# Kernel optimization log

Hardware: AMD Instinct MI355X
Metric: run time of the kernel (lower is better)

Reference implementation:

```python
import jax, jax.numpy as jnp
import numpy as np

DIM = 1024
D_STATE = 16
D_CONV = 4
EXPAND = 2
D_INNER = EXPAND * DIM          # 2048
DT_RANK = (DIM + 15) // 16      # 64 (math.ceil(d_model/16))
BSZ = 2
SEQ = 2048


def setup_inputs() -> dict:
    key = jax.random.key(0)
    ks = jax.random.split(key, 8)
    g = lambda k, shape, scale: (jax.random.normal(k, shape, jnp.float32) * scale)
    return {
        "x": g(ks[0], (BSZ, SEQ, DIM), 1.0),
        # in_proj: Linear(d_model -> 2*d_inner, bias=False)
        "W_in": g(ks[1], (2 * D_INNER, DIM), DIM ** -0.5),
        # depthwise causal conv1d: groups=d_inner, kernel d_conv, bias=True
        "conv_w": g(ks[2], (D_INNER, 1, D_CONV), D_CONV ** -0.5),
        "conv_b": jnp.zeros((D_INNER,), jnp.float32),
        # x_proj: Linear(d_inner -> dt_rank + 2*d_state, bias=False)
        "W_xproj": g(ks[3], (DT_RANK + 2 * D_STATE, D_INNER), D_INNER ** -0.5),
        # dt_proj: Linear(dt_rank -> d_inner, bias=True)
        "W_dt": g(ks[4], (D_INNER, DT_RANK), DT_RANK ** -0.5),
        "b_dt": g(ks[5], (D_INNER,), 0.1),
        # S4D-real init: A = -exp(A_log), A_log = log(1..d_state)
        "A_log": jnp.log(jnp.broadcast_to(
            jnp.arange(1, D_STATE + 1, dtype=jnp.float32), (D_INNER, D_STATE))),
        "D": jnp.ones((D_INNER,), jnp.float32),
        # out_proj: Linear(d_inner -> d_model, bias=False)
        "W_out": g(ks[6], (DIM, D_INNER), D_INNER ** -0.5),
        # wrapper LayerNorm(dim)
        "gamma": jnp.ones((DIM,), jnp.float32),
        "beta": jnp.zeros((DIM,), jnp.float32),
    }


def reference(x, W_in, conv_w, conv_b, W_xproj, W_dt, b_dt,
              A_log, D, W_out, gamma, beta):
    B, L, _ = x.shape
    # ---- input projection, split into conv path and gate ----
    xz = x @ W_in.T                              # (B, L, 2*d_inner)
    xc, z = jnp.split(xz, 2, axis=-1)
    # ---- depthwise causal conv1d + SiLU ----
    xt = jnp.transpose(xc, (0, 2, 1))            # (B, d_inner, L)
    conv = jax.lax.conv_general_dilated(
        xt, conv_w, window_strides=(1,), padding=[(D_CONV - 1, 0)],
        dimension_numbers=("NCH", "OIH", "NCH"), feature_group_count=D_INNER)
    u = jax.nn.silu(jnp.transpose(conv + conv_b[None, :, None], (0, 2, 1)))  # (B,L,d_inner)
    # ---- input-dependent delta, B, C ----
    xdbc = u @ W_xproj.T                          # (B, L, dt_rank + 2*d_state)
    dt = xdbc[..., :DT_RANK]
    Bm = xdbc[..., DT_RANK:DT_RANK + D_STATE]     # (B, L, d_state)
    Cm = xdbc[..., DT_RANK + D_STATE:]            # (B, L, d_state)
    delta = jax.nn.softplus(dt @ W_dt.T + b_dt)   # (B, L, d_inner)
    A = -jnp.exp(A_log)                           # (d_inner, d_state)
    # ---- selective scan: h_t = exp(dt*A) h_{t-1} + dt*B_t*u_t ; y_t = <h_t, C_t> ----
    def step(h, inputs):
        d_t, u_t, B_t, C_t = inputs               # (B,d_inner),(B,d_inner),(B,S),(B,S)
        dA = jnp.exp(d_t[:, :, None] * A)         # (B, d_inner, S)
        h = h * dA + (d_t * u_t)[:, :, None] * B_t[:, None, :]
        y = jnp.einsum("bds,bs->bd", h, C_t)
        return h, y
    tm = lambda a: jnp.transpose(a, (1, 0, 2))    # time-major for scan
    h0 = jnp.zeros((B, D_INNER, D_STATE), x.dtype)
    _, ys = jax.lax.scan(step, h0, (tm(delta), tm(u), tm(Bm), tm(Cm)))
    y = jnp.transpose(ys, (1, 0, 2)) + u * D      # skip term D*u
    y = y * jax.nn.silu(z)                        # gate
    out = y @ W_out.T                             # (B, L, dim)
    # ---- wrapper LayerNorm(dim), eps=1e-5 ----
    mean = out.mean(-1, keepdims=True)
    var = out.var(-1, keepdims=True)
    return (out - mean) * jax.lax.rsqrt(var + 1e-5) * gamma + beta
```

## Files before the change

### kernel.cpp

```cpp
#include <hip/hip_runtime.h>
#include <stdint.h>

typedef unsigned short u16;
typedef __bf16 bf16x8 __attribute__((ext_vector_type(8)));
typedef unsigned short u16x8 __attribute__((ext_vector_type(8)));
typedef unsigned short u16x4 __attribute__((ext_vector_type(4)));
typedef float f32x4 __attribute__((ext_vector_type(4)));

#define BSZ 2
#define SEQ 2048
#define DIM 1024
#define D_INNER 2048
#define DT_RANK 64
#define D_STATE 16
#define XPROJ_N 96
#define NCHUNK 32
#define CHUNK_T 64
#define LOG2E 1.44269504f

#define N_X   4194304
#define N_W   4194304
#define N_WX  196608
#define N_WDT 131072
#define N_WO  2097152
#define N_XD  393216

__device__ __forceinline__ float bf2f(u16 h) {
    return __uint_as_float(((unsigned)h) << 16);
}
__device__ __forceinline__ u16 f2bf(float f) {
    unsigned u = __float_as_uint(f);
    unsigned r = (u + 0x7FFFu + ((u >> 16) & 1u)) >> 16;
    return (u16)r;
}

__device__ __forceinline__ f32x4 mfma16(bf16x8 a, bf16x8 b, f32x4 c) {
    return __builtin_amdgcn_mfma_f32_16x16x32_bf16(a, b, c, 0, 0, 0);
}

__device__ __forceinline__ void gload_lds16(const void* g, void* l) {
    __builtin_amdgcn_global_load_lds(
        (const __attribute__((address_space(1))) unsigned int*)(uintptr_t)g,
        (__attribute__((address_space(3))) unsigned int*)(uintptr_t)l,
        16, 0, 0);
}

__device__ __forceinline__ void split4(const float* __restrict__ in,
                                       u16* __restrict__ hi, u16* __restrict__ lo,
                                       long i)
{
    f32x4 v = *(const f32x4*)(in + i);
    u16x4 h, l;
    #pragma unroll
    for (int j = 0; j < 4; j++) {
        u16 hh = f2bf(v[j]);
        h[j] = hh;
        l[j] = f2bf(v[j] - bf2f(hh));
    }
    *(u16x4*)(hi + i) = h;
    *(u16x4*)(lo + i) = l;
}

__global__ __launch_bounds__(256)
void megasplit4(const float* __restrict__ x,  u16* __restrict__ xh,  u16* __restrict__ xl,
                const float* __restrict__ w,  u16* __restrict__ wh,  u16* __restrict__ wl,
                const float* __restrict__ wx, u16* __restrict__ wxh, u16* __restrict__ wxl,
                const float* __restrict__ wd, u16* __restrict__ wdh, u16* __restrict__ wdl)
{
    long i = ((long)blockIdx.x * 256 + threadIdx.x) * 4;
    if (i < N_X) { split4(x, xh, xl, i); return; }
    i -= N_X;
    if (i < N_W) { split4(w, wh, wl, i); return; }
    i -= N_W;
    if (i < N_WX) { split4(wx, wxh, wxl, i); return; }
    i -= N_WX;
    if (i < N_WDT) { split4(wd, wdh, wdl, i); }
}

#define PH_TOP                                                                \
    __builtin_amdgcn_sched_barrier(0);                                        \
    __builtin_amdgcn_s_barrier();                                             \
    asm volatile("s_waitcnt lgkmcnt(0)" ::: "memory");                        \
    __builtin_amdgcn_sched_barrier(0);                                        \
    __builtin_amdgcn_s_setprio(1);
#define PH_BOT                                                                \
    __builtin_amdgcn_s_setprio(0);                                            \
    __builtin_amdgcn_sched_barrier(0);                                        \
    __builtin_amdgcn_s_barrier();

__global__ __launch_bounds__(512, 2)
void gemm256_xz(const u16* __restrict__ xh, const u16* __restrict__ xl,
                const u16* __restrict__ wh, const u16* __restrict__ wl,
                u16* __restrict__ xc, float* __restrict__ z)
{
    __shared__ u16 lds[65536];

    const int tid  = threadIdx.x;
    const int w    = tid >> 6;
    const int lane = tid & 63;
    const int r16  = lane & 15;
    const int quad = lane >> 4;
    const int wr   = w >> 2;
    const int wc   = w & 3;
    const long m0  = (long)blockIdx.y * 256;
    const long n0  = (long)blockIdx.x * 256;

    const int c0 = tid, c1 = tid + 512;
    const int ma0 = c0 >> 2, kc0 = ((c0 & 3) ^ ((ma0 >> 1) & 3)) * 8;
    const int ma1 = c1 >> 2, kc1 = ((c1 & 3) ^ ((ma1 >> 1) & 3)) * 8;
    const int arow0 = ((int)m0 + ma0) * DIM + kc0;
    const int arow1 = ((int)m0 + ma1) * DIM + kc1;
    const int brow0 = ((int)n0 + ma0) * DIM + kc0;
    const int brow1 = ((int)n0 + ma1) * DIM + kc1;

    int caof[8], cbof[4];
    #pragma unroll
    for (int i = 0; i < 8; i++) {
        int m = wr * 128 + i * 16 + r16;
        caof[i] = (m * 4 + (quad ^ ((m >> 1) & 3))) * 8;
    }
    #pragma unroll
    for (int j = 0; j < 4; j++) {
        int n = wc * 64 + j * 16 + r16;
        cbof[j] = (n * 4 + (quad ^ ((n >> 1) & 3))) * 8;
    }

    f32x4 acc[8][4];
    #pragma unroll
    for (int i = 0; i < 8; i++)
        #pragma unroll
        for (int j = 0; j < 4; j++) acc[i][j] = {0.f, 0.f, 0.f, 0.f};

    gload_lds16(xh + arow0, lds + c0 * 8);
    gload_lds16(xh + arow1, lds + c1 * 8);
    gload_lds16(xl + arow0, lds + 8192 + c0 * 8);
    gload_lds16(xl + arow1, lds + 8192 + c1 * 8);
    gload_lds16(wh + brow0, lds + 16384 + c0 * 8);
    gload_lds16(wh + brow1, lds + 16384 + c1 * 8);
    gload_lds16(wl + brow0, lds + 24576 + c0 * 8);
    gload_lds16(wl + brow1, lds + 24576 + c1 * 8);
    asm volatile("s_waitcnt vmcnt(0)" ::: "memory");
    __builtin_amdgcn_s_barrier();

    int kt = 0;
#define XZ_FTILE(CUR, SN)                                                     \
  {                                                                           \
    int st = kt + 1; if (st > 31) st = 31;                                    \
    const int kb = st * 32;                                                   \
    const u16* AHp = lds + (CUR) * 32768;                                     \
    const u16* ALp = AHp + 8192;                                              \
    const u16* BHp = AHp + 16384;                                             \
    const u16* BLp = AHp + 24576;                                             \
    u16* Sb = lds + (SN) * 32768;                                             \
    bf16x8 a0[4], a1[4], fb[4];                                               \
                            \
    _Pragma("unroll") for (int j = 0; j < 4; j++)                             \
        fb[j] = *(const bf16x8*)(BHp + cbof[j]);                              \
    _Pragma("unroll") for (int i = 0; i < 4; i++)                             \
        a0[i] = *(const bf16x8*)(AHp + caof[i]);                              \
    gload_lds16(xh + arow0 + kb, Sb + c0 * 8);                                \
    gload_lds16(xh + arow1 + kb, Sb + c1 * 8);                                \
    PH_TOP                                                                    \
    _Pragma("unroll") for (int i = 0; i < 4; i++)                             \
      _Pragma("unroll") for (int j = 0; j < 4; j++)                           \
        acc[i][j] = mfma16(a0[i], fb[j], acc[i][j]);                          \
    PH_BOT                                                                    \
                                \
    _Pragma("unroll") for (int i = 0; i < 4; i++)                             \
        a1[i] = *(const bf16x8*)(AHp + caof[4 + i]);                          \
    gload_lds16(xl + arow0 + kb, Sb + 8192 + c0 * 8);                         \
    gload_lds16(xl + arow1 + kb, Sb + 8192 + c1 * 8);                         \
    PH_TOP                                                                    \
    _Pragma("unroll") for (int i = 0; i < 4; i++)                             \
      _Pragma("unroll") for (int j = 0; j < 4; j++)                           \
        acc[4 + i][j] = mfma16(a1[i], fb[j], acc[4 + i][j]);                  \
    PH_BOT                                                                    \
                        \
    _Pragma("unroll") for (int j = 0; j < 4; j++)                             \
        fb[j] = *(const bf16x8*)(BLp + cbof[j]);                              \
    gload_lds16(wh + brow0 + kb, Sb + 16384 + c0 * 8);                        \
    gload_lds16(wh + brow1 + kb, Sb + 16384 + c1 * 8);                        \
    PH_TOP                                                                    \
    _Pragma("unroll") for (int i = 0; i < 4; i++)                             \
      _Pragma("unroll") for (int j = 0; j < 4; j++)                           \
        acc[i][j] = mfma16(a0[i], fb[j], acc[i][j]);                          \
    PH_BOT                                                                    \
                             \
    gload_lds16(wl + brow0 + kb, Sb + 24576 + c0 * 8);                        \
    gload_lds16(wl + brow1 + kb, Sb + 24576 + c1 * 8);                        \
    PH_TOP                                                                    \
    _Pragma("unroll") for (int i = 0; i < 4; i++)                             \
      _Pragma("unroll") for (int j = 0; j < 4; j++)                           \
        acc[4 + i][j] = mfma16(a1[i], fb[j], acc[4 + i][j]);                  \
    PH_BOT                                                                    \
                              \
    _Pragma("unroll") for (int j = 0; j < 4; j++)                             \
        fb[j] = *(const bf16x8*)(BHp + cbof[j]);                              \
    _Pragma("unroll") for (int i = 0; i < 4; i++)                             \
        a0[i] = *(const bf16x8*)(ALp + caof[i]);                              \
    PH_TOP                                                                    \
    _Pragma("unroll") for (int i = 0; i < 4; i++)                             \
      _Pragma("unroll") for (int j = 0; j < 4; j++)                           \
        acc[i][j] = mfma16(a0[i], fb[j], acc[i][j]);                          \
    PH_BOT                                                                    \
                 \
    _Pragma("unroll") for (int i = 0; i < 4; i++)                             \
        a1[i] = *(const bf16x8*)(ALp + caof[4 + i]);                          \
    PH_TOP                                                                    \
    _Pragma("unroll") for (int i = 0; i < 4; i++)                             \
      _Pragma("unroll") for (int j = 0; j < 4; j++)                           \
        acc[4 + i][j] = mfma16(a1[i], fb[j], acc[4 + i][j]);                  \
    __builtin_amdgcn_s_setprio(0);                                            \
    __builtin_amdgcn_sched_barrier(0);                                        \
    asm volatile("s_waitcnt vmcnt(0)" ::: "memory");                          \
    __builtin_amdgcn_s_barrier();                                             \
    kt++;                                                                     \
  }

    #pragma unroll 1
    for (int it = 0; it < 16; it++) {
        XZ_FTILE(0, 1)
        XZ_FTILE(1, 0)
    }
#undef XZ_FTILE

    asm volatile("s_waitcnt vmcnt(0)" ::: "memory");

    const bool isz = (n0 >= 2048);
    #pragma unroll
    for (int i = 0; i < 8; i++) {
        #pragma unroll
        for (int j = 0; j < 4; j++) {
            long col = n0 + wc * 64 + j * 16 + r16;
            #pragma unroll
            for (int r = 0; r < 4; r++) {
                long row = m0 + wr * 128 + i * 16 + quad * 4 + r;
                if (!isz) xc[row * (long)D_INNER + col] = f2bf(acc[i][j][r]);
                else      z[row * (long)D_INNER + (col - D_INNER)] = acc[i][j][r];
            }
        }
    }
}

__global__ __launch_bounds__(512, 2)
void gemm256_out(const u16* __restrict__ A, const u16* __restrict__ Bh,
                 const u16* __restrict__ Bl, float* __restrict__ OutBase)
{
    __shared__ u16 lds[49152];

    const int tid  = threadIdx.x;
    const int w    = tid >> 6;
    const int lane = tid & 63;
    const int r16  = lane & 15;
    const int quad = lane >> 4;
    const int wr   = w >> 2;
    const int wc   = w & 3;
    const long m0  = (long)blockIdx.y * 256;
    const long n0  = (long)blockIdx.x * 256;
    const int  kz  = blockIdx.z;
    const u16* Bs  = (kz >= 2) ? Bl : Bh;
    const int  kbase = (kz & 1) * 1024;
    float* Out = OutBase + (long)kz * 4194304;

    const int c0 = tid, c1 = tid + 512;
    const int ma0 = c0 >> 2, kc0 = ((c0 & 3) ^ ((ma0 >> 1) & 3)) * 8;
    const int ma1 = c1 >> 2, kc1 = ((c1 & 3) ^ ((ma1 >> 1) & 3)) * 8;
    const int arow0 = ((int)m0 + ma0) * D_INNER + kbase + kc0;
    const int arow1 = ((int)m0 + ma1) * D_INNER + kbase + kc1;
    const int brow0 = ((int)n0 + ma0) * D_INNER + kbase + kc0;
    const int brow1 = ((int)n0 + ma1) * D_INNER + kbase + kc1;

    int caof[8], cbof[4];
    #pragma unroll
    for (int i = 0; i < 8; i++) {
        int m = wr * 128 + i * 16 + r16;
        caof[i] = (m * 4 + (quad ^ ((m >> 1) & 3))) * 8;
    }
    #pragma unroll
    for (int j = 0; j < 4; j++) {
        int n = wc * 64 + j * 16 + r16;
        cbof[j] = (n * 4 + (quad ^ ((n >> 1) & 3))) * 8;
    }

    f32x4 acc[8][4];
    #pragma unroll
    for (int i = 0; i < 8; i++)
        #pragma unroll
        for (int j = 0; j < 4; j++) acc[i][j] = {0.f, 0.f, 0.f, 0.f};

    gload_lds16(A  + arow0,      lds + c0 * 8);
    gload_lds16(A  + arow1,      lds + c1 * 8);
    gload_lds16(Bs + brow0,      lds + 24576 + c0 * 8);
    gload_lds16(Bs + brow1,      lds + 24576 + c1 * 8);
    gload_lds16(A  + arow0 + 32, lds + 8192 + c0 * 8);
    gload_lds16(A  + arow1 + 32, lds + 8192 + c1 * 8);
    gload_lds16(Bs + brow0 + 32, lds + 24576 + 8192 + c0 * 8);
    gload_lds16(Bs + brow1 + 32, lds + 24576 + 8192 + c1 * 8);
    asm volatile("s_waitcnt vmcnt(4)" ::: "memory");
    __builtin_amdgcn_s_barrier();

    int kt = 0;
#define OUT_ITER(CUR, SL)                                                     \
  {                                                                           \
    int st = kt + 2; if (st > 31) st = 31;                                    \
    const int kb = st * 32;                                                   \
    const u16* Alds = lds + (CUR) * 8192;                                     \
    const u16* Blds = lds + 24576 + (CUR) * 8192;                             \
    bf16x8 bfr[4], afr[4];                                                    \
    _Pragma("unroll") for (int j = 0; j < 4; j++)                             \
        bfr[j] = *(const bf16x8*)(Blds + cbof[j]);                            \
    _Pragma("unroll") for (int i = 0; i < 4; i++)                             \
        afr[i] = *(const bf16x8*)(Alds + caof[i]);                            \
    gload_lds16(A + arow0 + kb, lds + (SL) * 8192 + c0 * 8);                  \
    gload_lds16(A + arow1 + kb, lds + (SL) * 8192 + c1 * 8);                  \
    PH_TOP                                                                    \
    _Pragma("unroll") for (int i = 0; i < 4; i++)                             \
      _Pragma("unroll") for (int j = 0; j < 4; j++)                           \
        acc[i][j] = mfma16(afr[i], bfr[j], acc[i][j]);                        \
    PH_BOT                                                                    \
    bf16x8 af2[4];                                                            \
    _Pragma("unroll") for (int i = 0; i < 4; i++)                             \
        af2[i] = *(const bf16x8*)(Alds + caof[4 + i]);                        \
    gload_lds16(Bs + brow0 + kb, lds + 24576 + (SL) * 8192 + c0 * 8);         \
    gload_lds16(Bs + brow1 + kb, lds + 24576 + (SL) * 8192 + c1 * 8);         \
    PH_TOP                                                                    \
    _Pragma("unroll") for (int i = 0; i < 4; i++)                             \
      _Pragma("unroll") for (int j = 0; j < 4; j++)                           \
        acc[4 + i][j] = mfma16(af2[i], bfr[j], acc[4 + i][j]);                \
    __builtin_amdgcn_s_setprio(0);                                            \
    __builtin_amdgcn_sched_barrier(0);                                        \
    asm volatile("s_waitcnt vmcnt(4)" ::: "memory");                          \
    __builtin_amdgcn_s_barrier();                                             \
    kt++;                                                                     \
  }

    #pragma unroll 1
    for (int it = 0; it < 10; it++) {
        OUT_ITER(0, 2)
        OUT_ITER(1, 0)
        OUT_ITER(2, 1)
    }
    OUT_ITER(0, 2)
    OUT_ITER(1, 0)
#undef OUT_ITER

    asm volatile("s_waitcnt vmcnt(0)" ::: "memory");

    #pragma unroll
    for (int i = 0; i < 8; i++) {
        #pragma unroll
        for (int j = 0; j < 4; j++) {
            long col = n0 + wc * 64 + j * 16 + r16;
            #pragma unroll
            for (int r = 0; r < 4; r++) {
                long row = m0 + wr * 128 + i * 16 + quad * 4 + r;
                Out[row * (long)DIM + col] = acc[i][j][r];
            }
        }
    }
}

__global__ __launch_bounds__(64)
void gemm_dt32(const u16* __restrict__ Ah, const u16* __restrict__ Al, int lda,
               const u16* __restrict__ Bh, const u16* __restrict__ Bl, int ldb,
               float* __restrict__ C, int ldc, const float* __restrict__ bias)
{
    const int lane = threadIdx.x;
    const int r16  = lane & 15;
    const int quad = lane >> 4;
    const long m0 = (long)blockIdx.y * 32;
    const long n0 = (long)blockIdx.x * 32;

    const u16* Ah0 = Ah + (m0 + r16) * (long)lda + quad * 8;
    const u16* Ah1 = Ah0 + 16L * lda;
    const u16* Al0 = Al + (m0 + r16) * (long)lda + quad * 8;
    const u16* Al1 = Al0 + 16L * lda;
    const u16* Bh0 = Bh + (n0 + r16) * (long)ldb + quad * 8;
    const u16* Bh1 = Bh0 + 16L * ldb;
    const u16* Bl0 = Bl + (n0 + r16) * (long)ldb + quad * 8;
    const u16* Bl1 = Bl0 + 16L * ldb;

    f32x4 acc00 = {0,0,0,0}, acc01 = {0,0,0,0}, acc10 = {0,0,0,0}, acc11 = {0,0,0,0};

    #pragma unroll
    for (int k = 0; k < DT_RANK; k += 32) {
        bf16x8 a0h = *(const bf16x8*)(Ah0 + k);
        bf16x8 a1h = *(const bf16x8*)(Ah1 + k);
        bf16x8 a0l = *(const bf16x8*)(Al0 + k);
        bf16x8 a1l = *(const bf16x8*)(Al1 + k);
        bf16x8 b0h = *(const bf16x8*)(Bh0 + k);
        bf16x8 b1h = *(const bf16x8*)(Bh1 + k);
        bf16x8 b0l = *(const bf16x8*)(Bl0 + k);
        bf16x8 b1l = *(const bf16x8*)(Bl1 + k);
        acc00 = mfma16(a0h, b0h, acc00); acc00 = mfma16(a0h, b0l, acc00); acc00 = mfma16(a0l, b0h, acc00);
        acc01 = mfma16(a0h, b1h, acc01); acc01 = mfma16(a0h, b1l, acc01); acc01 = mfma16(a0l, b1h, acc01);
        acc10 = mfma16(a1h, b0h, acc10); acc10 = mfma16(a1h, b0l, acc10); acc10 = mfma16(a1l, b0h, acc10);
        acc11 = mfma16(a1h, b1h, acc11); acc11 = mfma16(a1h, b1l, acc11); acc11 = mfma16(a1l, b1h, acc11);
    }

    #pragma unroll
    for (int i = 0; i < 2; i++) {
        #pragma unroll
        for (int j = 0; j < 2; j++) {
            f32x4 v = (i == 0) ? (j == 0 ? acc00 : acc01) : (j == 0 ? acc10 : acc11);
            long col = n0 + j * 16 + r16;
            #pragma unroll
            for (int r = 0; r < 4; r++) {
                long row = m0 + i * 16 + quad * 4 + r;
                float x = v[r] + bias[col];
                x = (x > 15.f) ? x : log1pf(__expf(x));
                C[row * (long)ldc + col] = x;
            }
        }
    }
}

__global__ __launch_bounds__(64)
void gemm3_skp(const u16* __restrict__ A, int lda,
               const u16* __restrict__ Bh, const u16* __restrict__ Bl, int ldb,
               float* __restrict__ Cpart, int ldc, int K0)
{
    const int lane = threadIdx.x;
    const int r16  = lane & 15;
    const int quad = lane >> 4;
    const long m0 = (long)blockIdx.y * 32;
    const long n0 = (long)blockIdx.x * 32;
    const int kbase = blockIdx.z * K0;
    float* C = Cpart + (long)blockIdx.z * N_XD;

    const u16* Ap0 = A  + (m0 + r16) * (long)lda + quad * 8 + kbase;
    const u16* Ap1 = Ap0 + 16L * lda;
    const u16* Bh0 = Bh + (n0 + r16) * (long)ldb + quad * 8 + kbase;
    const u16* Bh1 = Bh0 + 16L * ldb;
    const u16* Bl0 = Bl + (n0 + r16) * (long)ldb + quad * 8 + kbase;
    const u16* Bl1 = Bl0 + 16L * ldb;

    f32x4 acc00 = {0,0,0,0}, acc01 = {0,0,0,0}, acc10 = {0,0,0,0}, acc11 = {0,0,0,0};

    for (int k = 0; k < K0; k += 32) {
        bf16x8 a0 = *(const bf16x8*)(Ap0 + k);
        bf16x8 a1 = *(const bf16x8*)(Ap1 + k);
        bf16x8 b0h = *(const bf16x8*)(Bh0 + k);
        bf16x8 b1h = *(const bf16x8*)(Bh1 + k);
        bf16x8 b0l = *(const bf16x8*)(Bl0 + k);
        bf16x8 b1l = *(const bf16x8*)(Bl1 + k);
        acc00 = mfma16(a0, b0h, acc00); acc00 = mfma16(a0, b0l, acc00);
        acc01 = mfma16(a0, b1h, acc01); acc01 = mfma16(a0, b1l, acc01);
        acc10 = mfma16(a1, b0h, acc10); acc10 = mfma16(a1, b0l, acc10);
        acc11 = mfma16(a1, b1h, acc11); acc11 = mfma16(a1, b1l, acc11);
    }

    #pragma unroll
    for (int i = 0; i < 2; i++) {
        #pragma unroll
        for (int j = 0; j < 2; j++) {
            f32x4 v = (i == 0) ? (j == 0 ? acc00 : acc01) : (j == 0 ? acc10 : acc11);
            long col = n0 + j * 16 + r16;
            #pragma unroll
            for (int r = 0; r < 4; r++) {
                long row = m0 + i * 16 + quad * 4 + r;
                C[row * (long)ldc + col] = v[r];
            }
        }
    }
}

__global__ __launch_bounds__(256)
void combine3(const float* __restrict__ part, float* __restrict__ xdbc,
              u16* __restrict__ hi, u16* __restrict__ lo)
{
    long i = ((long)blockIdx.x * 256 + threadIdx.x) * 4;
    if (i >= N_XD) return;
    f32x4 s = *(const f32x4*)(part + i);
    #pragma unroll
    for (int j = 1; j < 8; j++) {
        f32x4 p = *(const f32x4*)(part + (long)j * N_XD + i);
        s[0] += p[0]; s[1] += p[1]; s[2] += p[2]; s[3] += p[3];
    }
    *(f32x4*)(xdbc + i) = s;
    u16x4 h, l;
    #pragma unroll
    for (int j = 0; j < 4; j++) {
        u16 hh = f2bf(s[j]);
        h[j] = hh;
        l[j] = f2bf(s[j] - bf2f(hh));
    }
    *(u16x4*)(hi + i) = h;
    *(u16x4*)(lo + i) = l;
}

__global__ __launch_bounds__(256)
void conv_silu(const u16* __restrict__ xc, const float* __restrict__ cw,
               const float* __restrict__ cb, u16* __restrict__ u)
{
    long idx = ((long)blockIdx.x * 256 + threadIdx.x) * 8;
    int t  = (int)((idx >> 11) & 2047);
    int d0 = (int)(idx & 2047);

    bf16x8 xrow[4];
    #pragma unroll
    for (int j = 0; j < 4; j++) {
        int tt = t - 3 + j;
        if (tt >= 0) xrow[j] = *(const bf16x8*)(xc + idx + (long)(j - 3) * D_INNER);
        else         xrow[j] = bf16x8{0,0,0,0,0,0,0,0};
    }
    u16x8 out;
    #pragma unroll
    for (int e = 0; e < 8; e++) {
        int d = d0 + e;
        float acc = cb[d];
        #pragma unroll
        for (int j = 0; j < 4; j++)
            acc += cw[d * 4 + j] * (float)xrow[j][e];
        out[e] = f2bf(acc / (1.f + __expf(-acc)));
    }
    *(u16x8*)(u + idx) = out;
}

__global__ __launch_bounds__(256)
void scan_partA(const float* __restrict__ delta, const u16* __restrict__ u,
                const float* __restrict__ xdbc, const float* __restrict__ A_log,
                float* __restrict__ hbuf, float* __restrict__ sdelta,
                const float* __restrict__ wout, u16* __restrict__ wouth,
                u16* __restrict__ woutl)
{
    const int d = blockIdx.x * 256 + threadIdx.x;
    const int c = blockIdx.y;
    const int b = blockIdx.z;
    const int t0 = c * CHUNK_T;

    float Af[16];
    #pragma unroll
    for (int s = 0; s < 16; s++) Af[s] = -__expf(A_log[d * 16 + s]) * LOG2E;

    float h[16];
    #pragma unroll
    for (int s = 0; s < 16; s++) h[s] = 0.f;
    float sd = 0.f;

    const float* dptr = delta + ((long)b * SEQ + t0) * D_INNER + d;
    const u16*   uptr = u     + ((long)b * SEQ + t0) * D_INNER + d;
    const float* xp   = xdbc  + ((long)b * SEQ + t0) * XPROJ_N;

    for (int t = 0; t < CHUNK_T; t++) {
        float dl = dptr[(long)t * D_INNER];
        float uu = bf2f(uptr[(long)t * D_INNER]);
        f32x4 B0 = *(const f32x4*)(xp + t * XPROJ_N + DT_RANK);
        f32x4 B1 = *(const f32x4*)(xp + t * XPROJ_N + DT_RANK + 4);
        f32x4 B2 = *(const f32x4*)(xp + t * XPROJ_N + DT_RANK + 8);
        f32x4 B3 = *(const f32x4*)(xp + t * XPROJ_N + DT_RANK + 12);
        float Bv[16] = {B0[0],B0[1],B0[2],B0[3], B1[0],B1[1],B1[2],B1[3],
                        B2[0],B2[1],B2[2],B2[3], B3[0],B3[1],B3[2],B3[3]};
        sd += dl;
        float dlu = dl * uu;
        #pragma unroll
        for (int s = 0; s < 16; s++)
            h[s] = h[s] * exp2f(dl * Af[s]) + dlu * Bv[s];
    }

    float* hout = hbuf + ((long)(b * NCHUNK + c) * D_INNER + d) * 16;
    #pragma unroll
    for (int s = 0; s < 16; s++) hout[s] = h[s];
    sdelta[(long)(b * NCHUNK + c) * D_INNER + d] = sd;

    long tidg = (((long)b * NCHUNK + c) * 8 + blockIdx.x) * 256 + threadIdx.x;
    long base = tidg * 16;
    #pragma unroll
    for (int k = 0; k < 4; k++) split4(wout, wouth, woutl, base + 4 * k);
}

__global__ __launch_bounds__(256)
void scan_fixup(float* __restrict__ hbuf, const float* __restrict__ sdelta,
                const float* __restrict__ A_log)
{
    const int idx = blockIdx.x * 256 + threadIdx.x;
    const int ds = idx & (D_INNER * 16 - 1);
    const int b  = idx >> 15;
    const float Af = -__expf(A_log[ds]) * LOG2E;
    float hin = 0.f;
    #pragma unroll 4
    for (int c = 0; c < NCHUNK; c++) {
        long gi = (long)(b * NCHUNK + c) * (D_INNER * 16) + ds;
        float e = hbuf[gi];
        hbuf[gi] = hin;
        float sd = sdelta[(long)(b * NCHUNK + c) * D_INNER + (ds >> 4)];
        hin = e + exp2f(Af * sd) * hin;
    }
}

__global__ __launch_bounds__(256)
void scan_partC(const float* __restrict__ delta, const u16* __restrict__ u,
                const float* __restrict__ xdbc, const float* __restrict__ z,
                const float* __restrict__ A_log, const float* __restrict__ Dp,
                const float* __restrict__ hbuf, u16* __restrict__ y)
{
    const int d = blockIdx.x * 256 + threadIdx.x;
    const int c = blockIdx.y;
    const int b = blockIdx.z;
    const int t0 = c * CHUNK_T;

    float Af[16];
    #pragma unroll
    for (int s = 0; s < 16; s++) Af[s] = -__expf(A_log[d * 16 + s]) * LOG2E;
    const float Dd = Dp[d];

    float h[16];
    const float* hin = hbuf + ((long)(b * NCHUNK + c) * D_INNER + d) * 16;
    #pragma unroll
    for (int s = 0; s < 16; s++) h[s] = hin[s];

    const float* dptr = delta + ((long)b * SEQ + t0) * D_INNER + d;
    const u16*   uptr = u     + ((long)b * SEQ + t0) * D_INNER + d;
    const float* zptr = z     + ((long)b * SEQ + t0) * D_INNER + d;
    const float* xp   = xdbc  + ((long)b * SEQ + t0) * XPROJ_N;
    u16* yptr = y + ((long)b * SEQ + t0) * D_INNER + d;

    for (int t = 0; t < CHUNK_T; t++) {
        float dl = dptr[(long)t * D_INNER];
        float uu = bf2f(uptr[(long)t * D_INNER]);
        float zl = zptr[(long)t * D_INNER];
        f32x4 B0 = *(const f32x4*)(xp + t * XPROJ_N + DT_RANK);
        f32x4 B1 = *(const f32x4*)(xp + t * XPROJ_N + DT_RANK + 4);
        f32x4 B2 = *(const f32x4*)(xp + t * XPROJ_N + DT_RANK + 8);
        f32x4 B3 = *(const f32x4*)(xp + t * XPROJ_N + DT_RANK + 12);
        f32x4 C0 = *(const f32x4*)(xp + t * XPROJ_N + DT_RANK + 16);
        f32x4 C1 = *(const f32x4*)(xp + t * XPROJ_N + DT_RANK + 20);
        f32x4 C2 = *(const f32x4*)(xp + t * XPROJ_N + DT_RANK + 24);
        f32x4 C3 = *(const f32x4*)(xp + t * XPROJ_N + DT_RANK + 28);
        float Bv[16] = {B0[0],B0[1],B0[2],B0[3], B1[0],B1[1],B1[2],B1[3],
                        B2[0],B2[1],B2[2],B2[3], B3[0],B3[1],B3[2],B3[3]};
        float Cv[16] = {C0[0],C0[1],C0[2],C0[3], C1[0],C1[1],C1[2],C1[3],
                        C2[0],C2[1],C2[2],C2[3], C3[0],C3[1],C3[2],C3[3]};
        float dlu = dl * uu;
        float p0 = 0.f, p1 = 0.f, p2 = 0.f, p3 = 0.f;
        #pragma unroll
        for (int s = 0; s < 16; s += 4) {
            h[s]   = h[s]   * exp2f(dl * Af[s])   + dlu * Bv[s];
            h[s+1] = h[s+1] * exp2f(dl * Af[s+1]) + dlu * Bv[s+1];
            h[s+2] = h[s+2] * exp2f(dl * Af[s+2]) + dlu * Bv[s+2];
            h[s+3] = h[s+3] * exp2f(dl * Af[s+3]) + dlu * Bv[s+3];
            p0 += h[s]   * Cv[s];
            p1 += h[s+1] * Cv[s+1];
            p2 += h[s+2] * Cv[s+2];
            p3 += h[s+3] * Cv[s+3];
        }
        float acc = (p0 + p1) + (p2 + p3);
        float sz = zl / (1.f + __expf(-zl));
        float yy = (acc + uu * Dd) * sz;
        yptr[(long)t * D_INNER] = f2bf(yy);
    }
}

__global__ __launch_bounds__(256)
void layernorm_kernel(const float* __restrict__ p0,
                      const float* __restrict__ gamma, const float* __restrict__ beta,
                      float* __restrict__ out)
{
    const long row = blockIdx.x;
    const long base = row * DIM;
    int tid = threadIdx.x;
    float v[4];
    float sum = 0.f, sq = 0.f;
    #pragma unroll
    for (int i = 0; i < 4; i++) {
        long c = base + tid + i * 256;
        v[i] = (p0[c] + p0[c + 4194304]) + (p0[c + 8388608] + p0[c + 12582912]);
        sum += v[i];
        sq  += v[i] * v[i];
    }
    #pragma unroll
    for (int off = 1; off < 64; off <<= 1) {
        sum += __shfl_xor(sum, off);
        sq  += __shfl_xor(sq, off);
    }
    __shared__ float ssum[4], ssq[4];
    int w = tid >> 6;
    if ((tid & 63) == 0) { ssum[w] = sum; ssq[w] = sq; }
    __syncthreads();
    float ts = ssum[0] + ssum[1] + ssum[2] + ssum[3];
    float tq = ssq[0] + ssq[1] + ssq[2] + ssq[3];
    float mean = ts * (1.f / DIM);
    float var  = tq * (1.f / DIM) - mean * mean;
    float rstd = rsqrtf(var + 1e-5f);
    float* o = out + base;
    #pragma unroll
    for (int i = 0; i < 4; i++) {
        int c = tid + i * 256;
        o[c] = (v[i] - mean) * rstd * gamma[c] + beta[c];
    }
}

extern "C" void kernel_launch(void* const* d_in, const int* in_sizes, int n_in,
                              void* d_out, int out_size, void* d_ws, size_t ws_size,
                              hipStream_t stream)
{
    const float* x      = (const float*)d_in[0];
    const float* W_in   = (const float*)d_in[1];
    const float* conv_w = (const float*)d_in[2];
    const float* conv_b = (const float*)d_in[3];
    const float* W_xproj= (const float*)d_in[4];
    const float* W_dt   = (const float*)d_in[5];
    const float* b_dt   = (const float*)d_in[6];
    const float* A_log  = (const float*)d_in[7];
    const float* Dv     = (const float*)d_in[8];
    const float* W_out  = (const float*)d_in[9];
    const float* gamma  = (const float*)d_in[10];
    const float* beta   = (const float*)d_in[11];

    char* ws = (char*)d_ws;
    u16*   xc    = (u16*)(ws);
    float* g3p   = (float*)(ws);
    u16*   xdh   = (u16*)(ws + 12582912);
    u16*   xdl   = (u16*)(ws + 14155776);
    float* hbuf  = (float*)(ws);
    u16*   wouth = (u16*)(ws + 8388608);
    u16*   woutl = (u16*)(ws + 12582912);
    float* z     = (float*)(ws + 16777216);
    float* opre  = (float*)(ws + 16777216);
    u16*   u     = (u16*)(ws + 50331648);
    u16*   xh    = (u16*)(ws + 67108864);
    u16*   xl    = (u16*)(ws + 75497472);
    u16*   wh    = (u16*)(ws + 83886080);
    u16*   wl    = (u16*)(ws + 92274688);
    float* delta = (float*)(ws + 67108864);
    float* xdbc  = (float*)(ws + 100663296);
    u16*   wxh   = (u16*)(ws + 102236160);
    u16*   wxl   = (u16*)(ws + 102629376);
    u16*   wdth  = (u16*)(ws + 103022592);
    u16*   wdtl  = (u16*)(ws + 103284736);
    float* sdel  = (float*)(ws + 103546880);
    u16*   yb    = (u16*)d_out;

    megasplit4<<<8512, 256, 0, stream>>>(x, xh, xl, W_in, wh, wl,
                                         W_xproj, wxh, wxl, W_dt, wdth, wdtl);
    gemm256_xz<<<dim3(16, 16), 512, 0, stream>>>(xh, xl, wh, wl, xc, z);
    conv_silu<<<4096, 256, 0, stream>>>(xc, conv_w, conv_b, u);
    gemm3_skp<<<dim3(3, 128, 8), 64, 0, stream>>>(
        u, D_INNER, wxh, wxl, D_INNER, g3p, XPROJ_N, 256);
    combine3<<<384, 256, 0, stream>>>(g3p, xdbc, xdh, xdl);
    gemm_dt32<<<dim3(64, 128), 64, 0, stream>>>(
        xdh, xdl, XPROJ_N, wdth, wdtl, DT_RANK, delta, D_INNER, b_dt);
    scan_partA<<<dim3(8, NCHUNK, BSZ), 256, 0, stream>>>(
        delta, u, xdbc, A_log, hbuf, sdel, W_out, wouth, woutl);
    scan_fixup<<<256, 256, 0, stream>>>(hbuf, sdel, A_log);
    scan_partC<<<dim3(8, NCHUNK, BSZ), 256, 0, stream>>>(delta, u, xdbc, z, A_log, Dv, hbuf, yb);
    gemm256_out<<<dim3(4, 16, 4), 512, 0, stream>>>(yb, wouth, woutl, opre);
    layernorm_kernel<<<4096, 256, 0, stream>>>(opre, gamma, beta, (float*)d_out);
}
```

Measured before the change: 429.6 us.

## Split scan state across thread pairs and merge MFMA phases in xz GEMM

The scan kernels now assign two threads per channel, each handling 8 of the 16 state dimensions, and combine the C-dot products with a lane shuffle. This doubles the grid to raise occupancy and cut per-thread serial work in the latency-bound recurrence, at the cost of duplicated delta/u/z loads. Separately, the xz GEMM inner tile merges pairs of MFMA phases, hoisting LDS fragment loads earlier and reducing priority toggles and scheduling barriers. The W_out split work is redistributed to match the new grid.

New measurement: 446.5 us. 4.0% more time.

```diff
diff --git a/kernel.cpp b/kernel.cpp
--- a/kernel.cpp
+++ b/kernel.cpp
@@ -153,7 +153,7 @@
     const u16* BLp = AHp + 24576;                                             \
     u16* Sb = lds + (SN) * 32768;                                             \
     bf16x8 a0[4], a1[4], fb[4];                                               \
-                            \
+                         \
     _Pragma("unroll") for (int j = 0; j < 4; j++)                             \
         fb[j] = *(const bf16x8*)(BHp + cbof[j]);                              \
     _Pragma("unroll") for (int i = 0; i < 4; i++)                             \
@@ -165,7 +165,7 @@
       _Pragma("unroll") for (int j = 0; j < 4; j++)                           \
         acc[i][j] = mfma16(a0[i], fb[j], acc[i][j]);                          \
     PH_BOT                                                                    \
-                                \
+                             \
     _Pragma("unroll") for (int i = 0; i < 4; i++)                             \
         a1[i] = *(const bf16x8*)(AHp + caof[4 + i]);                          \
     gload_lds16(xl + arow0 + kb, Sb + 8192 + c0 * 8);                         \
@@ -175,38 +175,32 @@
       _Pragma("unroll") for (int j = 0; j < 4; j++)                           \
         acc[4 + i][j] = mfma16(a1[i], fb[j], acc[4 + i][j]);                  \
     PH_BOT                                                                    \
-                        \
+                  \
     _Pragma("unroll") for (int j = 0; j < 4; j++)                             \
         fb[j] = *(const bf16x8*)(BLp + cbof[j]);                              \
     gload_lds16(wh + brow0 + kb, Sb + 16384 + c0 * 8);                        \
     gload_lds16(wh + brow1 + kb, Sb + 16384 + c1 * 8);                        \
-    PH_TOP                                                                    \
-    _Pragma("unroll") for (int i = 0; i < 4; i++)                             \
-      _Pragma("unroll") for (int j = 0; j < 4; j++)                           \
-        acc[i][j] = mfma16(a0[i], fb[j], acc[i][j]);                          \
-    PH_BOT                                                                    \
-                             \
     gload_lds16(wl + brow0 + kb, Sb + 24576 + c0 * 8);                        \
     gload_lds16(wl + brow1 + kb, Sb + 24576 + c1 * 8);                        \
     PH_TOP                                                                    \
     _Pragma("unroll") for (int i = 0; i < 4; i++)                             \
       _Pragma("unroll") for (int j = 0; j < 4; j++)                           \
+        acc[i][j] = mfma16(a0[i], fb[j], acc[i][j]);                          \
+    _Pragma("unroll") for (int i = 0; i < 4; i++)                             \
+      _Pragma("unroll") for (int j = 0; j < 4; j++)                           \
         acc[4 + i][j] = mfma16(a1[i], fb[j], acc[4 + i][j]);                  \
     PH_BOT                                                                    \
-                              \
+              \
     _Pragma("unroll") for (int j = 0; j < 4; j++)                             \
         fb[j] = *(const bf16x8*)(BHp + cbof[j]);                              \
     _Pragma("unroll") for (int i = 0; i < 4; i++)                             \
         a0[i] = *(const bf16x8*)(ALp + caof[i]);                              \
+    _Pragma("unroll") for (int i = 0; i < 4; i++)                             \
+        a1[i] = *(const bf16x8*)(ALp + caof[4 + i]);                          \
     PH_TOP                                                                    \
     _Pragma("unroll") for (int i = 0; i < 4; i++)                             \
       _Pragma("unroll") for (int j = 0; j < 4; j++)                           \
         acc[i][j] = mfma16(a0[i], fb[j], acc[i][j]);                          \
-    PH_BOT                                                                    \
-                 \
-    _Pragma("unroll") for (int i = 0; i < 4; i++)                             \
-        a1[i] = *(const bf16x8*)(ALp + caof[4 + i]);                          \
-    PH_TOP                                                                    \
     _Pragma("unroll") for (int i = 0; i < 4; i++)                             \
       _Pragma("unroll") for (int j = 0; j < 4; j++)                           \
         acc[4 + i][j] = mfma16(a1[i], fb[j], acc[4 + i][j]);                  \
@@ -524,18 +518,20 @@
                 const float* __restrict__ wout, u16* __restrict__ wouth,
                 u16* __restrict__ woutl)
 {
-    const int d = blockIdx.x * 256 + threadIdx.x;
+    const int tid = threadIdx.x;
+    const int d  = blockIdx.x * 128 + (tid >> 1);
+    const int sh = (tid & 1) * 8;
     const int c = blockIdx.y;
     const int b = blockIdx.z;
     const int t0 = c * CHUNK_T;
 
-    float Af[16];
-    #pragma unroll
-    for (int s = 0; s < 16; s++) Af[s] = -__expf(A_log[d * 16 + s]) * LOG2E;
-
-    float h[16];
-    #pragma unroll
-    for (int s = 0; s < 16; s++) h[s] = 0.f;
+    float Af[8];
+    #pragma unroll
+    for (int s = 0; s < 8; s++) Af[s] = -__expf(A_log[d * 16 + sh + s]) * LOG2E;
+
+    float h[8];
+    #pragma unroll
+    for (int s = 0; s < 8; s++) h[s] = 0.f;
     float sd = 0.f;
 
     const float* dptr = delta + ((long)b * SEQ + t0) * D_INNER + d;
@@ -545,28 +541,26 @@
     for (int t = 0; t < CHUNK_T; t++) {
         float dl = dptr[(long)t * D_INNER];
         float uu = bf2f(uptr[(long)t * D_INNER]);
-        f32x4 B0 = *(const f32x4*)(xp + t * XPROJ_N + DT_RANK);
-        f32x4 B1 = *(const f32x4*)(xp + t * XPROJ_N + DT_RANK + 4);
-        f32x4 B2 = *(const f32x4*)(xp + t * XPROJ_N + DT_RANK + 8);
-        f32x4 B3 = *(const f32x4*)(xp + t * XPROJ_N + DT_RANK + 12);
-        float Bv[16] = {B0[0],B0[1],B0[2],B0[3], B1[0],B1[1],B1[2],B1[3],
-                        B2[0],B2[1],B2[2],B2[3], B3[0],B3[1],B3[2],B3[3]};
+        f32x4 B0 = *(const f32x4*)(xp + t * XPROJ_N + DT_RANK + sh);
+        f32x4 B1 = *(const f32x4*)(xp + t * XPROJ_N + DT_RANK + sh + 4);
+        float Bv[8] = {B0[0],B0[1],B0[2],B0[3], B1[0],B1[1],B1[2],B1[3]};
         sd += dl;
         float dlu = dl * uu;
         #pragma unroll
-        for (int s = 0; s < 16; s++)
+        for (int s = 0; s < 8; s++)
             h[s] = h[s] * exp2f(dl * Af[s]) + dlu * Bv[s];
     }
 
-    float* hout = hbuf + ((long)(b * NCHUNK + c) * D_INNER + d) * 16;
-    #pragma unroll
-    for (int s = 0; s < 16; s++) hout[s] = h[s];
-    sdelta[(long)(b * NCHUNK + c) * D_INNER + d] = sd;
-
-    long tidg = (((long)b * NCHUNK + c) * 8 + blockIdx.x) * 256 + threadIdx.x;
-    long base = tidg * 16;
-    #pragma unroll
-    for (int k = 0; k < 4; k++) split4(wout, wouth, woutl, base + 4 * k);
+    float* hout = hbuf + ((long)(b * NCHUNK + c) * D_INNER + d) * 16 + sh;
+    #pragma unroll
+    for (int s = 0; s < 8; s++) hout[s] = h[s];
+    if (!(tid & 1))
+        sdelta[(long)(b * NCHUNK + c) * D_INNER + d] = sd;
+
+    long tidg = (((long)b * NCHUNK + c) * 16 + blockIdx.x) * 256 + tid;
+    long base = tidg * 8;
+    split4(wout, wouth, woutl, base);
+    split4(wout, wouth, woutl, base + 4);
 }
 
 __global__ __launch_bounds__(256)
@@ -594,20 +588,22 @@
                 const float* __restrict__ A_log, const float* __restrict__ Dp,
                 const float* __restrict__ hbuf, u16* __restrict__ y)
 {
-    const int d = blockIdx.x * 256 + threadIdx.x;
+    const int tid = threadIdx.x;
+    const int d  = blockIdx.x * 128 + (tid >> 1);
+    const int sh = (tid & 1) * 8;
     const int c = blockIdx.y;
     const int b = blockIdx.z;
     const int t0 = c * CHUNK_T;
 
-    float Af[16];
-    #pragma unroll
-    for (int s = 0; s < 16; s++) Af[s] = -__expf(A_log[d * 16 + s]) * LOG2E;
+    float Af[8];
+    #pragma unroll
+    for (int s = 0; s < 8; s++) Af[s] = -__expf(A_log[d * 16 + sh + s]) * LOG2E;
     const float Dd = Dp[d];
 
-    float h[16];
-    const float* hin = hbuf + ((long)(b * NCHUNK + c) * D_INNER + d) * 16;
-    #pragma unroll
-    for (int s = 0; s < 16; s++) h[s] = hin[s];
+    float h[8];
+    const float* hin = hbuf + ((long)(b * NCHUNK + c) * D_INNER + d) * 16 + sh;
+    #pragma unroll
+    for (int s = 0; s < 8; s++) h[s] = hin[s];
 
     const float* dptr = delta + ((long)b * SEQ + t0) * D_INNER + d;
     const u16*   uptr = u     + ((long)b * SEQ + t0) * D_INNER + d;
@@ -619,22 +615,16 @@
         float dl = dptr[(long)t * D_INNER];
         float uu = bf2f(uptr[(long)t * D_INNER]);
         float zl = zptr[(long)t * D_INNER];
-        f32x4 B0 = *(const f32x4*)(xp + t * XPROJ_N + DT_RANK);
-        f32x4 B1 = *(const f32x4*)(xp + t * XPROJ_N + DT_RANK + 4);
-        f32x4 B2 = *(const f32x4*)(xp + t * XPROJ_N + DT_RANK + 8);
-        f32x4 B3 = *(const f32x4*)(xp + t * XPROJ_N + DT_RANK + 12);
-        f32x4 C0 = *(const f32x4*)(xp + t * XPROJ_N + DT_RANK + 16);
-        f32x4 C1 = *(const f32x4*)(xp + t * XPROJ_N + DT_RANK + 20);
-        f32x4 C2 = *(const f32x4*)(xp + t * XPROJ_N + DT_RANK + 24);
-        f32x4 C3 = *(const f32x4*)(xp + t * XPROJ_N + DT_RANK + 28);
-        float Bv[16] = {B0[0],B0[1],B0[2],B0[3], B1[0],B1[1],B1[2],B1[3],
-                        B2[0],B2[1],B2[2],B2[3], B3[0],B3[1],B3[2],B3[3]};
-        float Cv[16] = {C0[0],C0[1],C0[2],C0[3], C1[0],C1[1],C1[2],C1[3],
-                        C2[0],C2[1],C2[2],C2[3], C3[0],C3[1],C3[2],C3[3]};
+        f32x4 B0 = *(const f32x4*)(xp + t * XPROJ_N + DT_RANK + sh);
+        f32x4 B1 = *(const f32x4*)(xp + t * XPROJ_N + DT_RANK + sh + 4);
+        f32x4 C0 = *(const f32x4*)(xp + t * XPROJ_N + DT_RANK + 16 + sh);
+        f32x4 C1 = *(const f32x4*)(xp + t * XPROJ_N + DT_RANK + 16 + sh + 4);
+        float Bv[8] = {B0[0],B0[1],B0[2],B0[3], B1[0],B1[1],B1[2],B1[3]};
+        float Cv[8] = {C0[0],C0[1],C0[2],C0[3], C1[0],C1[1],C1[2],C1[3]};
         float dlu = dl * uu;
         float p0 = 0.f, p1 = 0.f, p2 = 0.f, p3 = 0.f;
         #pragma unroll
-        for (int s = 0; s < 16; s += 4) {
+        for (int s = 0; s < 8; s += 4) {
             h[s]   = h[s]   * exp2f(dl * Af[s])   + dlu * Bv[s];
             h[s+1] = h[s+1] * exp2f(dl * Af[s+1]) + dlu * Bv[s+1];
             h[s+2] = h[s+2] * exp2f(dl * Af[s+2]) + dlu * Bv[s+2];
@@ -644,10 +634,11 @@
             p2 += h[s+2] * Cv[s+2];
             p3 += h[s+3] * Cv[s+3];
         }
-        float acc = (p0 + p1) + (p2 + p3);
+        float accp = (p0 + p1) + (p2 + p3);
+        float acc = accp + __shfl_xor(accp, 1);
         float sz = zl / (1.f + __expf(-zl));
         float yy = (acc + uu * Dd) * sz;
-        yptr[(long)t * D_INNER] = f2bf(yy);
+        if (!(tid & 1)) yptr[(long)t * D_INNER] = f2bf(yy);
     }
 }
 
@@ -740,10 +731,10 @@
     combine3<<<384, 256, 0, stream>>>(g3p, xdbc, xdh, xdl);
     gemm_dt32<<<dim3(64, 128), 64, 0, stream>>>(
         xdh, xdl, XPROJ_N, wdth, wdtl, DT_RANK, delta, D_INNER, b_dt);
-    scan_partA<<<dim3(8, NCHUNK, BSZ), 256, 0, stream>>>(
+    scan_partA<<<dim3(16, NCHUNK, BSZ), 256, 0, stream>>>(
         delta, u, xdbc, A_log, hbuf, sdel, W_out, wouth, woutl);
     scan_fixup<<<256, 256, 0, stream>>>(hbuf, sdel, A_log);
-    scan_partC<<<dim3(8, NCHUNK, BSZ), 256, 0, stream>>>(delta, u, xdbc, z, A_log, Dv, hbuf, yb);
+    scan_partC<<<dim3(16, NCHUNK, BSZ), 256, 0, stream>>>(delta, u, xdbc, z, A_log, Dv, hbuf, yb);
     gemm256_out<<<dim3(4, 16, 4), 512, 0, stream>>>(yb, wouth, woutl, opre);
     layernorm_kernel<<<4096, 256, 0, stream>>>(opre, gamma, beta, (float*)d_out);
 }
```
